# Kernel optimization log

Hardware: AMD Instinct MI355X
Metric: run time of the kernel (lower is better)

## Reference

```python
import jax, jax.numpy as jnp
import numpy as np

B, S, DIN, DOUT, R, NL, T = 4, 4096, 1024, 1024, 16, 8, 4

def setup_inputs() -> dict:
    key = jax.random.key(0)
    k1, k2, k3, k4, k5 = jax.random.split(key, 5)
    return {
        "x": jax.random.normal(k1, (B, S, DIN), dtype=jnp.float32),
        "W": jax.random.normal(k2, (DOUT, DIN), dtype=jnp.float32) * 0.02,
        "bias": jax.random.normal(k3, (DOUT,), dtype=jnp.float32) * 0.02,
        "lora_A": jax.random.normal(k4, (NL, R, DIN), dtype=jnp.float32) * 0.02,
        "lora_B": jax.random.normal(k5, (NL, DOUT, R), dtype=jnp.float32) * 0.02,
        "tuner_index": jnp.arange(T, dtype=jnp.int64) if jax.config.jax_enable_x64 else jnp.arange(T, dtype=jnp.int32),
    }

def reference(x, W, bias, lora_A, lora_B, tuner_index):
    # Per adapter ti: F.linear(x, W + B_ti @ A_ti, bias)
    # == x @ W.T + (x @ A_ti.T) @ B_ti.T + bias  (fused low-rank form, same math)
    A = lora_A[tuner_index]   # [T, r, Din]
    Bm = lora_B[tuner_index]  # [T, Dout, r]
    base = jnp.einsum('bsd,od->bso', x, W) + bias          # [B, S, Dout]
    low = jnp.einsum('bsd,trd->tbsr', x, A)                # [T, B, S, r]
    delta = jnp.einsum('tbsr,tor->tbso', low, Bm)          # [T, B, S, Dout]
    return base[None, ...] + delta                         # [T, B, S, Dout]
```

## Files before the change

### kernel.cpp

```cpp
#include <hip/hip_runtime.h>


typedef __attribute__((ext_vector_type(8))) _Float16 f16x8;
typedef __attribute__((ext_vector_type(4))) float f32x4;
typedef __attribute__((ext_vector_type(4))) unsigned short us4;
typedef __attribute__((ext_vector_type(8))) unsigned short us8;

namespace {
constexpr int kM = 16384, kDin = 1024, kDout = 1024, kR = 16, kT = 4;
constexpr size_t OFF_XF  = 0;
constexpr size_t OFF_WF  = 33554432;
constexpr size_t OFF_LOW = 35651584;
}

__device__ inline unsigned short f2h(float f) {
  _Float16 h = (_Float16)f;
  return __builtin_bit_cast(unsigned short, h);
}
__device__ inline void gload_lds16(const void* g, void* l) {
  __builtin_amdgcn_global_load_lds(
      (const __attribute__((address_space(1))) unsigned int*)g,
      (__attribute__((address_space(3))) unsigned int*)l, 16, 0, 0);
}
__device__ inline f32x4 mfma_f16(f16x8 a, f16x8 b, f32x4 c) {
  return __builtin_amdgcn_mfma_f32_16x16x32_f16(a, b, c, 0, 0, 0);
}

__global__ __launch_bounds__(256) void cvt_f16(const float* __restrict__ x,
                                               const float* __restrict__ W,
                                               unsigned short* __restrict__ xf,
                                               unsigned short* __restrict__ wf) {
  constexpr int NX4 = kM * kDin / 4;
  constexpr int NW4 = kDout * kDin / 4;
  const int stride = gridDim.x * blockDim.x;
  for (int i = blockIdx.x * blockDim.x + threadIdx.x; i < NX4 + NW4; i += stride) {
    const bool isx = i < NX4;
    const int  j   = isx ? i : i - NX4;
    const float4 v = isx ? ((const float4*)x)[j] : ((const float4*)W)[j];
    us4 h;
    h[0] = f2h(v.x); h[1] = f2h(v.y); h[2] = f2h(v.z); h[3] = f2h(v.w);
    if (isx) ((us4*)xf)[j] = h;
    else     ((us4*)wf)[j] = h;
  }
}

__global__ __launch_bounds__(256) void lora_low(const float* __restrict__ x,
                                                const float* __restrict__ A,
                                                const int* __restrict__ tuner,
                                                unsigned short* __restrict__ lowb) {
  __shared__ float xs[64][34];
  __shared__ float as[64][66];
  const int tid = threadIdx.x;
  const int i0  = blockIdx.x * 32;
  const int tx  = tid & 15;
  const int ty  = tid >> 4;
  float acc[2][4] = {{0.f, 0.f, 0.f, 0.f}, {0.f, 0.f, 0.f, 0.f}};

  for (int kt = 0; kt < kDin; kt += 64) {
    __syncthreads();
#pragma unroll
    for (int p = 0; p < 2; ++p) {
      const int f = tid + p * 256;
      const int row = f >> 4, kq = (f & 15) * 4;
      const float4 v = *(const float4*)(x + (size_t)(i0 + row) * kDin + kt + kq);
      xs[kq + 0][row] = v.x; xs[kq + 1][row] = v.y;
      xs[kq + 2][row] = v.z; xs[kq + 3][row] = v.w;
    }
#pragma unroll
    for (int p = 0; p < 4; ++p) {
      const int f = tid + p * 256;
      const int ar = f >> 4, kq = (f & 15) * 4;
      const int ti = tuner[ar >> 4];
      const float4 v = *(const float4*)(A + ((size_t)ti * kR + (ar & 15)) * kDin + kt + kq);
      as[kq + 0][ar] = v.x; as[kq + 1][ar] = v.y;
      as[kq + 2][ar] = v.z; as[kq + 3][ar] = v.w;
    }
    __syncthreads();
#pragma unroll 8
    for (int k = 0; k < 64; ++k) {
      const float a0 = xs[k][ty * 2], a1 = xs[k][ty * 2 + 1];
      const float b0 = as[k][tx * 4], b1 = as[k][tx * 4 + 1];
      const float b2 = as[k][tx * 4 + 2], b3 = as[k][tx * 4 + 3];
      acc[0][0] += a0 * b0; acc[0][1] += a0 * b1; acc[0][2] += a0 * b2; acc[0][3] += a0 * b3;
      acc[1][0] += a1 * b0; acc[1][1] += a1 * b1; acc[1][2] += a1 * b2; acc[1][3] += a1 * b3;
    }
  }
#pragma unroll
  for (int ii = 0; ii < 2; ++ii) {
    us4 o;
#pragma unroll
    for (int j = 0; j < 4; ++j) o[j] = f2h(acc[ii][j]);
    *(us4*)(lowb + ((size_t)(tx >> 2) * kM + i0 + ty * 2 + ii) * kR + (tx & 3) * 4) = o;
  }
}

__global__ __launch_bounds__(256) void lora_main(
    const unsigned short* __restrict__ xf, const unsigned short* __restrict__ wf,
    const float* __restrict__ bias, const float* __restrict__ Bm,
    const int* __restrict__ tuner, const unsigned short* __restrict__ lowb,
    float* __restrict__ out) {
  __shared__ __align__(16) unsigned char smem[32768];
  const int tid  = threadIdx.x;
  const int lane = tid & 63;
  const int w    = tid >> 6;

  const int swz = ((int)blockIdx.x & 7) * 128 + ((int)blockIdx.x >> 3);
  const int bm = swz >> 3, bn = swz & 7;
  const size_t i0 = (size_t)bm * 128, j0 = (size_t)bn * 128;
  const int wm = w >> 1, wn = w & 1;

  const int wp = w & 1;
  const unsigned short* gsrc = (w < 2) ? xf : wf;
  const size_t grow0 = ((w < 2) ? i0 : j0) + wp * 64;
  const unsigned short* gbase =
      gsrc + (grow0 + (lane >> 2)) * kDin + ((lane & 3) ^ ((lane >> 3) & 3)) * 8;
  const int stoff = (w >> 1) * 8192 + wp * 4096;

  f32x4 acc[4][4];
#pragma unroll
  for (int m = 0; m < 4; ++m)
#pragma unroll
    for (int n = 0; n < 4; ++n) acc[m][n] = (f32x4){0.f, 0.f, 0.f, 0.f};

  const int kg = lane >> 4;
  const int rl = lane & 15;
  const int csw = kg ^ ((rl >> 1) & 3);
  const int rdA = (wm * 64 + rl) * 64 + csw * 16;
  const int rdB = 8192 + (wn * 64 + rl) * 64 + csw * 16;

  auto compute_step = [&](const unsigned char* B0) {
    f16x8 a[4], b[4];
#pragma unroll
    for (int m = 0; m < 4; ++m) {
      a[m] = *(const f16x8*)(B0 + rdA + m * 1024);
      b[m] = *(const f16x8*)(B0 + rdB + m * 1024);
    }
    __builtin_amdgcn_s_setprio(1);
#pragma unroll
    for (int m = 0; m < 4; ++m)
#pragma unroll
      for (int n = 0; n < 4; ++n)
        acc[m][n] = mfma_f16(a[m], b[n], acc[m][n]);
    __builtin_amdgcn_s_setprio(0);
  };

  {
    unsigned char* dst = smem + stoff;
#pragma unroll
    for (int c = 0; c < 4; ++c)
      gload_lds16(gbase + c * 16 * kDin, dst + c * 1024);
  }

  for (int s = 0; s < 31; ++s) {
    const int p = s & 1;
    {
      unsigned char* dst = smem + (p ^ 1) * 16384 + stoff;
      const unsigned short* src = gbase + (s + 1) * 32;
#pragma unroll
      for (int c = 0; c < 4; ++c)
        gload_lds16(src + c * 16 * kDin, dst + c * 1024);
    }
    asm volatile("s_waitcnt vmcnt(4)" ::: "memory");
    __builtin_amdgcn_s_barrier();
    asm volatile("" ::: "memory");
    compute_step(smem + p * 16384);
    asm volatile("s_waitcnt lgkmcnt(0)" ::: "memory");
    __builtin_amdgcn_s_barrier();
    asm volatile("" ::: "memory");
  }
  asm volatile("s_waitcnt vmcnt(0)" ::: "memory");
  __builtin_amdgcn_s_barrier();
  asm volatile("" ::: "memory");
  compute_step(smem + 16384);

  float bv[4];
#pragma unroll
  for (int n = 0; n < 4; ++n) bv[n] = bias[j0 + wn * 64 + n * 16 + rl];
#pragma unroll
  for (int m = 0; m < 4; ++m)
#pragma unroll
    for (int n = 0; n < 4; ++n)
#pragma unroll
      for (int r = 0; r < 4; ++r) acc[m][n][r] += bv[n];

  {
    unsigned char* p = (tid < 128) ? (smem + 4096 + tid * 32)
                                   : (smem + 12288 + (tid - 128) * 32);
    const us8 z = {0, 0, 0, 0, 0, 0, 0, 0};
    *(us8*)p = z;
    *(us8*)(p + 16) = z;
  }

  for (int t = 0; t < kT; ++t) {
    __syncthreads();
    {
      const int row = tid >> 1, half = tid & 1;
      const us8 lv = *(const us8*)(lowb + ((size_t)t * kM + i0 + row) * kR + half * 8);
      *(us8*)(smem + half * 2048 + row * 16) = lv;
      const int ti = tuner[t];
      const float* bp = Bm + ((size_t)ti * kDout + j0 + row) * kR + half * 8;
      const float4 m0 = *(const float4*)bp;
      const float4 m1 = *(const float4*)(bp + 4);
      us8 mv;
      mv[0] = f2h(m0.x); mv[1] = f2h(m0.y); mv[2] = f2h(m0.z); mv[3] = f2h(m0.w);
      mv[4] = f2h(m1.x); mv[5] = f2h(m1.y); mv[6] = f2h(m1.z); mv[7] = f2h(m1.w);
      *(us8*)(smem + 8192 + half * 2048 + row * 16) = mv;
    }
    __syncthreads();

    f16x8 lf[4], mf[4];
#pragma unroll
    for (int m = 0; m < 4; ++m)
      lf[m] = *(const f16x8*)(smem + kg * 2048 + (wm * 64 + m * 16 + rl) * 16);
#pragma unroll
    for (int n = 0; n < 4; ++n)
      mf[n] = *(const f16x8*)(smem + 8192 + kg * 2048 + (wn * 64 + n * 16 + rl) * 16);

#pragma unroll
    for (int m = 0; m < 4; ++m)
#pragma unroll
      for (int n = 0; n < 4; ++n) {
        const f32x4 d = mfma_f16(lf[m], mf[n], acc[m][n]);
        const int r4  = wm * 64 + m * 16 + kg * 4;
        const int col = (int)j0 + wn * 64 + n * 16 + rl;
        const size_t base = ((size_t)t * kM + i0 + r4) * kDout + col;
        out[base]             = d[0];
        out[base + kDout]     = d[1];
        out[base + 2 * kDout] = d[2];
        out[base + 3 * kDout] = d[3];
      }
  }
}

extern "C" void kernel_launch(void* const* d_in, const int* in_sizes, int n_in,
                              void* d_out, int out_size, void* d_ws, size_t ws_size,
                              hipStream_t stream) {
  const float* x    = (const float*)d_in[0];
  const float* W    = (const float*)d_in[1];
  const float* bias = (const float*)d_in[2];
  const float* lA   = (const float*)d_in[3];
  const float* lB   = (const float*)d_in[4];
  const int*   ti   = (const int*)d_in[5];
  float* out = (float*)d_out;

  unsigned char* ws = (unsigned char*)d_ws;
  unsigned short* xfp  = (unsigned short*)(ws + OFF_XF);
  unsigned short* wfp  = (unsigned short*)(ws + OFF_WF);
  unsigned short* lowb = (unsigned short*)(ws + OFF_LOW);

  cvt_f16<<<1024, 256, 0, stream>>>(x, W, xfp, wfp);
  lora_low<<<kM / 32, 256, 0, stream>>>(x, lA, ti, lowb);
  lora_main<<<1024, 256, 0, stream>>>(xfp, wfp, bias, lB, ti, lowb, out);
}
```

Measured before the change: 168.2 us.

## Fuse x fp16 conversion into lora_low and store output via transposed MFMA

The fp32-to-fp16 conversion of x now happens inside lora_low, which already reads x. This removes one full extra read pass over the 64MB x tensor and leaves a small W-only conversion kernel. The MFMA operands in the main kernel are also swapped (B×A) so each lane holds four contiguous output columns. That lets the epilogue write float4 vector stores instead of strided scalar stores, and the bias load becomes a vector load as well. The cost is that lora_low now carries the extra fp16 stores of x.

```diff
diff --git a/kernel.cpp b/kernel.cpp
--- a/kernel.cpp
+++ b/kernel.cpp
@@ -26,28 +26,23 @@
   return __builtin_amdgcn_mfma_f32_16x16x32_f16(a, b, c, 0, 0, 0);
 }
 
-__global__ __launch_bounds__(256) void cvt_f16(const float* __restrict__ x,
-                                               const float* __restrict__ W,
-                                               unsigned short* __restrict__ xf,
-                                               unsigned short* __restrict__ wf) {
-  constexpr int NX4 = kM * kDin / 4;
+__global__ __launch_bounds__(256) void cvt_W(const float* __restrict__ W,
+                                             unsigned short* __restrict__ wf) {
   constexpr int NW4 = kDout * kDin / 4;
   const int stride = gridDim.x * blockDim.x;
-  for (int i = blockIdx.x * blockDim.x + threadIdx.x; i < NX4 + NW4; i += stride) {
-    const bool isx = i < NX4;
-    const int  j   = isx ? i : i - NX4;
-    const float4 v = isx ? ((const float4*)x)[j] : ((const float4*)W)[j];
+  for (int j = blockIdx.x * blockDim.x + threadIdx.x; j < NW4; j += stride) {
+    const float4 v = ((const float4*)W)[j];
     us4 h;
     h[0] = f2h(v.x); h[1] = f2h(v.y); h[2] = f2h(v.z); h[3] = f2h(v.w);
-    if (isx) ((us4*)xf)[j] = h;
-    else     ((us4*)wf)[j] = h;
+    ((us4*)wf)[j] = h;
   }
 }
 
 __global__ __launch_bounds__(256) void lora_low(const float* __restrict__ x,
                                                 const float* __restrict__ A,
                                                 const int* __restrict__ tuner,
-                                                unsigned short* __restrict__ lowb) {
+                                                unsigned short* __restrict__ lowb,
+                                                unsigned short* __restrict__ xf) {
   __shared__ float xs[64][34];
   __shared__ float as[64][66];
   const int tid = threadIdx.x;
@@ -65,6 +60,9 @@
       const float4 v = *(const float4*)(x + (size_t)(i0 + row) * kDin + kt + kq);
       xs[kq + 0][row] = v.x; xs[kq + 1][row] = v.y;
       xs[kq + 2][row] = v.z; xs[kq + 3][row] = v.w;
+      us4 h;
+      h[0] = f2h(v.x); h[1] = f2h(v.y); h[2] = f2h(v.z); h[3] = f2h(v.w);
+      *(us4*)(xf + (size_t)(i0 + row) * kDin + kt + kq) = h;
     }
 #pragma unroll
     for (int p = 0; p < 4; ++p) {
@@ -118,9 +116,9 @@
 
   f32x4 acc[4][4];
 #pragma unroll
-  for (int m = 0; m < 4; ++m)
-#pragma unroll
-    for (int n = 0; n < 4; ++n) acc[m][n] = (f32x4){0.f, 0.f, 0.f, 0.f};
+  for (int n = 0; n < 4; ++n)
+#pragma unroll
+    for (int m = 0; m < 4; ++m) acc[n][m] = (f32x4){0.f, 0.f, 0.f, 0.f};
 
   const int kg = lane >> 4;
   const int rl = lane & 15;
@@ -137,10 +135,10 @@
     }
     __builtin_amdgcn_s_setprio(1);
 #pragma unroll
-    for (int m = 0; m < 4; ++m)
-#pragma unroll
-      for (int n = 0; n < 4; ++n)
-        acc[m][n] = mfma_f16(a[m], b[n], acc[m][n]);
+    for (int n = 0; n < 4; ++n)
+#pragma unroll
+      for (int m = 0; m < 4; ++m)
+        acc[n][m] = mfma_f16(b[n], a[m], acc[n][m]);
     __builtin_amdgcn_s_setprio(0);
   };
 
@@ -173,15 +171,14 @@
   asm volatile("" ::: "memory");
   compute_step(smem + 16384);
 
-  float bv[4];
-#pragma unroll
-  for (int n = 0; n < 4; ++n) bv[n] = bias[j0 + wn * 64 + n * 16 + rl];
-#pragma unroll
-  for (int m = 0; m < 4; ++m)
-#pragma unroll
-    for (int n = 0; n < 4; ++n)
-#pragma unroll
-      for (int r = 0; r < 4; ++r) acc[m][n][r] += bv[n];
+#pragma unroll
+  for (int n = 0; n < 4; ++n) {
+    const f32x4 bv = *(const f32x4*)(bias + j0 + wn * 64 + n * 16 + kg * 4);
+#pragma unroll
+    for (int m = 0; m < 4; ++m)
+#pragma unroll
+      for (int r = 0; r < 4; ++r) acc[n][m][r] += bv[r];
+  }
 
   {
     unsigned char* p = (tid < 128) ? (smem + 4096 + tid * 32)
@@ -217,17 +214,13 @@
       mf[n] = *(const f16x8*)(smem + 8192 + kg * 2048 + (wn * 64 + n * 16 + rl) * 16);
 
 #pragma unroll
-    for (int m = 0; m < 4; ++m)
-#pragma unroll
-      for (int n = 0; n < 4; ++n) {
-        const f32x4 d = mfma_f16(lf[m], mf[n], acc[m][n]);
-        const int r4  = wm * 64 + m * 16 + kg * 4;
-        const int col = (int)j0 + wn * 64 + n * 16 + rl;
-        const size_t base = ((size_t)t * kM + i0 + r4) * kDout + col;
-        out[base]             = d[0];
-        out[base + kDout]     = d[1];
-        out[base + 2 * kDout] = d[2];
-        out[base + 3 * kDout] = d[3];
+    for (int n = 0; n < 4; ++n)
+#pragma unroll
+      for (int m = 0; m < 4; ++m) {
+        const f32x4 d = mfma_f16(mf[n], lf[m], acc[n][m]);
+        const size_t row = (size_t)t * kM + i0 + wm * 64 + m * 16 + rl;
+        const int    col = (int)j0 + wn * 64 + n * 16 + kg * 4;
+        *(f32x4*)(out + row * kDout + col) = d;
       }
   }
 }
@@ -248,7 +241,7 @@
   unsigned short* wfp  = (unsigned short*)(ws + OFF_WF);
   unsigned short* lowb = (unsigned short*)(ws + OFF_LOW);
 
-  cvt_f16<<<1024, 256, 0, stream>>>(x, W, xfp, wfp);
-  lora_low<<<kM / 32, 256, 0, stream>>>(x, lA, ti, lowb);
+  cvt_W<<<64, 256, 0, stream>>>(W, wfp);
+  lora_low<<<kM / 32, 256, 0, stream>>>(x, lA, ti, lowb, xfp);
   lora_main<<<1024, 256, 0, stream>>>(xfp, wfp, bias, lB, ti, lowb, out);
 }
```

New measurement: 170.6 us. No clear change (+1.4%).
